# Kernel tuning notes

Hardware: AMD Instinct MI355X
Metric: run time of the kernel (lower is better)

The kernel has to match this reference:

```python
import jax, jax.numpy as jnp
import numpy as np

DIM = 128
WIN = (2, 7, 7)
HEADS = 4
N = WIN[0] * WIN[1] * WIN[2]  # 98
B_ = 2048
NW = 256  # num windows per sample; B_ // NW = batch = 8


def _relative_position_index(win):
    t = np.arange(win[0]); h = np.arange(win[1]); w = np.arange(win[2])
    coords = np.stack(np.meshgrid(t, h, w, indexing='ij'))  # (3, T, H, W)
    cf = coords.reshape(3, -1)  # (3, N)
    rel = cf[:, :, None] - cf[:, None, :]  # (3, N, N)
    rel = rel.transpose(1, 2, 0).copy()
    rel[:, :, 0] += win[0] - 1
    rel[:, :, 1] += win[1] - 1
    rel[:, :, 2] += win[2] - 1
    rel[:, :, 0] *= (2 * win[1] - 1) * (2 * win[2] - 1)
    rel[:, :, 1] *= 2 * win[2] - 1
    return rel.sum(-1).astype(np.int32)  # (N, N)


def setup_inputs() -> dict:
    key = jax.random.key(0)
    ks = jax.random.split(key, 8)
    table_len = (2 * WIN[0] - 1) * (2 * WIN[1] - 1) * (2 * WIN[2] - 1)  # 507
    x = jax.random.normal(ks[0], (B_, N, DIM), dtype=jnp.float32)
    # 0 / -inf style additive mask (use -1e4 as finite -inf)
    u = jax.random.uniform(ks[1], (NW, N, N))
    mask = jnp.where(u < 0.9, 0.0, -1e4).astype(jnp.float32)
    qkv_w = jax.random.normal(ks[2], (3 * DIM, DIM), dtype=jnp.float32) * (DIM ** -0.5)
    qkv_b = jax.random.normal(ks[3], (3 * DIM,), dtype=jnp.float32) * 0.02
    proj_w = jax.random.normal(ks[4], (DIM, DIM), dtype=jnp.float32) * (DIM ** -0.5)
    proj_b = jax.random.normal(ks[5], (DIM,), dtype=jnp.float32) * 0.02
    bias_table = jax.random.normal(ks[6], (table_len, HEADS), dtype=jnp.float32) * 0.02
    rel_index = jnp.asarray(_relative_position_index(WIN))
    return {"x": x, "mask": mask, "qkv_w": qkv_w, "qkv_b": qkv_b,
            "proj_w": proj_w, "proj_b": proj_b, "bias_table": bias_table,
            "rel_index": rel_index}


def reference(x, mask, qkv_w, qkv_b, proj_w, proj_b, bias_table, rel_index):
    Bq, n, c = x.shape
    hd = c // HEADS
    scale = hd ** -0.5
    qkv = x @ qkv_w.T + qkv_b  # (B_, N, 3C)
    qkv = qkv.reshape(Bq, n, 3, HEADS, hd).transpose(2, 0, 3, 1, 4)  # (3, B_, H, N, hd)
    q, k, v = qkv[0] * scale, qkv[1], qkv[2]
    attn = jnp.einsum('bhnd,bhmd->bhnm', q, k)  # (B_, H, N, N)
    bias = bias_table[rel_index.reshape(-1)].reshape(n, n, HEADS)
    attn = attn + bias.transpose(2, 0, 1)[None]  # add (1, H, N, N)
    nW = mask.shape[0]
    attn = attn.reshape(Bq // nW, nW, HEADS, n, n) + mask[None, :, None]
    attn = jax.nn.softmax(attn.reshape(Bq, HEADS, n, n), axis=-1)
    out = jnp.einsum('bhnm,bhmd->bhnd', attn, v)  # (B_, H, N, hd)
    out = out.transpose(0, 2, 1, 3).reshape(Bq, n, c)
    return out @ proj_w.T + proj_b
```

## Files before the change

kernel.cpp:

```cpp
#include <hip/hip_runtime.h>
#include <hip/hip_bf16.h>


#define NTOK 98
#define NN (NTOK * NTOK)
#define SCALE 0.17677669529663687f

typedef short bf16x8 __attribute__((ext_vector_type(8)));
typedef float f32x4 __attribute__((ext_vector_type(4)));
#define MFMA(a, b, c) __builtin_amdgcn_mfma_f32_16x16x32_bf16(a, b, c, 0, 0, 0)

static __device__ __forceinline__ unsigned short f2bf(float f) {
  union { float f; unsigned int i; } x; x.f = f;
  unsigned int u = x.i;
  unsigned int rnd = ((u >> 16) & 1u) + 0x7fffu;
  return (unsigned short)((u + rnd) >> 16);
}
static __device__ __forceinline__ float bf2f(short s) {
  union { unsigned int i; float f; } x;
  x.i = ((unsigned int)(unsigned short)s) << 16;
  return x.f;
}

__global__ void k0_w(const float* __restrict__ qkv_w, const float* __restrict__ proj_w,
                     unsigned short* __restrict__ wqb, unsigned short* __restrict__ wpb) {
  int idx = blockIdx.x * 256 + threadIdx.x;
  if (idx < 49152) wqb[idx] = f2bf(qkv_w[idx]);
  else wpb[idx - 49152] = f2bf(proj_w[idx - 49152]);
}

__global__ void k0b_bm(const float* __restrict__ table, const int* __restrict__ rel,
                       const float* __restrict__ mask, unsigned short* __restrict__ bm) {
  const int wmodh = blockIdx.x, mt = blockIdx.y;
  const int wmod = wmodh >> 2, h = wmodh & 3;
  const int t = threadIdx.x;
  const int lane = t >> 2, reg = t & 3;
  const int quad = lane >> 4, L15 = lane & 15;
  const int row = mt * 16 + quad * 4 + reg;
  bf16x8 v8;
#pragma unroll
  for (int nt = 0; nt < 8; ++nt) {
    float v = -1.0e30f;
    int col = nt * 16 + L15;
    if (nt < 7 && row < NTOK && col < NTOK) {
      int nm = row * NTOK + col;
      v = table[rel[nm] * 4 + h] + mask[(size_t)wmod * NN + nm];
    }
    v8[nt] = (short)f2bf(v);
  }
  *(bf16x8*)&bm[(((size_t)wmodh * 7 + mt) << 11) + (lane << 5) + (reg << 3)] = v8;
}

__global__ __launch_bounds__(256) void k1_qkv(const float* __restrict__ x,
                                              const unsigned short* __restrict__ wqb,
                                              const float* __restrict__ qkv_b,
                                              unsigned short* __restrict__ q,
                                              unsigned short* __restrict__ k,
                                              unsigned short* __restrict__ v) {
  __shared__ unsigned short xt[64 * 136];
  __shared__ unsigned short wt[128 * 136];
  const int t = threadIdx.x;
  const int r0 = blockIdx.x * 64;
  const int wv = t >> 6, lane = t & 63, L15 = lane & 15, quad = lane >> 4;

#pragma unroll
  for (int i = 0; i < 8; ++i) {
    int idx = t + (i << 8);
    int row = idx >> 5, c4 = idx & 31;
    float4 xv = *(const float4*)&x[(size_t)(r0 + row) * 128 + c4 * 4];
    ushort4 pk; pk.x = f2bf(xv.x); pk.y = f2bf(xv.y); pk.z = f2bf(xv.z); pk.w = f2bf(xv.w);
    *(ushort4*)&xt[row * 136 + c4 * 4] = pk;
  }

  bf16x8 af[4];
  bool afLoaded = false;

  for (int g = 0; g < 3; ++g) {
    if (g) __syncthreads();
#pragma unroll
    for (int i = 0; i < 8; ++i) {
      int idx = t + (i << 8);
      int c = idx >> 4, kq = idx & 15;
      *(uint4*)&wt[c * 136 + kq * 8] = ((const uint4*)wqb)[g * 2048 + idx];
    }
    __syncthreads();
    if (!afLoaded) {
      afLoaded = true;
#pragma unroll
      for (int kt = 0; kt < 4; ++kt)
        af[kt] = *(const bf16x8*)&xt[(wv * 16 + L15) * 136 + kt * 32 + quad * 8];
    }

    f32x4 acc[8];
#pragma unroll
    for (int nt = 0; nt < 8; ++nt) {
      f32x4 a = {0.f, 0.f, 0.f, 0.f};
#pragma unroll
      for (int kt = 0; kt < 4; ++kt) {
        bf16x8 bf_ = *(const bf16x8*)&wt[(nt * 16 + L15) * 136 + kt * 32 + quad * 8];
        a = MFMA(af[kt], bf_, a);
      }
      acc[nt] = a;
    }

    unsigned short* dst = (g == 0) ? q : ((g == 1) ? k : v);
    const float sc = (g == 0) ? SCALE : 1.0f;
    float bias[8];
#pragma unroll
    for (int nt = 0; nt < 8; ++nt) bias[nt] = qkv_b[g * 128 + nt * 16 + L15];
#pragma unroll
    for (int reg = 0; reg < 4; ++reg) {
      int R = r0 + wv * 16 + quad * 4 + reg;
      int b = R / NTOK, n = R - b * NTOK;
      size_t base0 = ((size_t)b * 4 * NTOK + n) * 32;
#pragma unroll
      for (int nt = 0; nt < 8; ++nt) {
        int h = nt >> 1, dd = ((nt & 1) << 4) + L15;
        float val = (acc[nt][reg] + bias[nt]) * sc;
        dst[base0 + (size_t)h * (NTOK * 32) + dd] = f2bf(val);
      }
    }
  }
}

__global__ __launch_bounds__(256) void k2_attn(const unsigned short* __restrict__ qg,
                                               const unsigned short* __restrict__ kg,
                                               const unsigned short* __restrict__ vg,
                                               const unsigned short* __restrict__ bm,
                                               unsigned short* __restrict__ og) {
  __shared__ unsigned short sK[112 * 40];
  __shared__ unsigned short sVt[32 * 136];
  __shared__ unsigned short sP[4 * 16 * 136];
  const int t = threadIdx.x;
  const int bh = blockIdx.x, bw = bh >> 2, h = bh & 3;
  const int wmodh = ((bw & 255) << 2) + h;
  const size_t base = (size_t)bh * (NTOK * 32);
  const int wv = t >> 6, lane = t & 63, L15 = lane & 15, quad = lane >> 4;
  unsigned short* myP = sP + wv * (16 * 136);

  for (int i = t; i < 2240; i += 256) ((unsigned int*)sK)[i] = 0;
  for (int j = lane; j < 128; j += 64) {
    int r = j >> 3, cp = j & 7;
    *(unsigned int*)&myP[r * 136 + 112 + cp * 2] = 0;
  }
  __syncthreads();
  for (int i = t; i < 392; i += 256) {
    int row = i >> 2, kq = i & 3;
    *(uint4*)&sK[row * 40 + kq * 8] = ((const uint4*)kg)[(size_t)bh * 392 + i];
  }
  for (int i = t; i < 3136; i += 256) {
    int n = i >> 5, d = i & 31;
    sVt[d * 136 + n] = vg[base + i];
  }
  __syncthreads();

  auto strip = [&](int mt) {
    const unsigned short* bmp = bm + (((size_t)wmodh * 7 + mt) << 11) + (lane << 5);
    bf16x8 bmv[4];
#pragma unroll
    for (int reg = 0; reg < 4; ++reg) bmv[reg] = *(const bf16x8*)&bmp[reg << 3];
    bf16x8 aq = *(const bf16x8*)&qg[base + (size_t)(mt * 16 + L15) * 32 + quad * 8];
    f32x4 s[7];
#pragma unroll
    for (int nt = 0; nt < 7; ++nt) {
      bf16x8 bk = *(const bf16x8*)&sK[(nt * 16 + L15) * 40 + quad * 8];
      f32x4 z = {0.f, 0.f, 0.f, 0.f};
      s[nt] = MFMA(aq, bk, z);
    }
#pragma unroll
    for (int reg = 0; reg < 4; ++reg) {
      float mx = -3.0e38f;
#pragma unroll
      for (int nt = 0; nt < 7; ++nt) {
        float val = s[nt][reg] + bf2f(bmv[reg][nt]);
        s[nt][reg] = val;
        mx = fmaxf(mx, val);
      }
#pragma unroll
      for (int d = 1; d < 16; d <<= 1) mx = fmaxf(mx, __shfl_xor(mx, d, 64));
      float sum = 0.f;
#pragma unroll
      for (int nt = 0; nt < 7; ++nt) {
        float e = __expf(s[nt][reg] - mx);
        s[nt][reg] = e; sum += e;
      }
#pragma unroll
      for (int d = 1; d < 16; d <<= 1) sum += __shfl_xor(sum, d, 64);
      float rs = 1.0f / sum;
#pragma unroll
      for (int nt = 0; nt < 7; ++nt)
        myP[(quad * 4 + reg) * 136 + nt * 16 + L15] = f2bf(s[nt][reg] * rs);
    }
    f32x4 o0 = {0.f, 0.f, 0.f, 0.f}, o1 = {0.f, 0.f, 0.f, 0.f};
#pragma unroll
    for (int kt = 0; kt < 4; ++kt) {
      bf16x8 ap  = *(const bf16x8*)&myP[L15 * 136 + kt * 32 + quad * 8];
      bf16x8 bv0 = *(const bf16x8*)&sVt[L15 * 136 + kt * 32 + quad * 8];
      bf16x8 bv1 = *(const bf16x8*)&sVt[(16 + L15) * 136 + kt * 32 + quad * 8];
      o0 = MFMA(ap, bv0, o0);
      o1 = MFMA(ap, bv1, o1);
    }
#pragma unroll
    for (int reg = 0; reg < 4; ++reg) {
      int n = mt * 16 + quad * 4 + reg;
      if (n < NTOK) {
        size_t ob = ((size_t)bw * NTOK + n) * 128 + h * 32;
        og[ob + L15]      = f2bf(o0[reg]);
        og[ob + 16 + L15] = f2bf(o1[reg]);
      }
    }
  };
  strip(wv * 2);
  if (wv < 3) strip(wv * 2 + 1);
}

__global__ __launch_bounds__(256) void k3_proj(const unsigned short* __restrict__ og,
                                               const unsigned short* __restrict__ wpb,
                                               const float* __restrict__ pb,
                                               float* __restrict__ out) {
  __shared__ unsigned short ot[64 * 136];
  __shared__ unsigned short wt[128 * 136];
  const int t = threadIdx.x;
  const int r0 = blockIdx.x * 64;
  const int wv = t >> 6, lane = t & 63, L15 = lane & 15, quad = lane >> 4;

#pragma unroll
  for (int i = 0; i < 4; ++i) {
    int idx = t + (i << 8);
    int row = idx >> 4, kq = idx & 15;
    *(uint4*)&ot[row * 136 + kq * 8] = ((const uint4*)og)[(size_t)(r0 + row) * 16 + kq];
  }
#pragma unroll
  for (int i = 0; i < 8; ++i) {
    int idx = t + (i << 8);
    int c = idx >> 4, kq = idx & 15;
    *(uint4*)&wt[c * 136 + kq * 8] = ((const uint4*)wpb)[idx];
  }
  __syncthreads();

  bf16x8 af[4];
#pragma unroll
  for (int kt = 0; kt < 4; ++kt)
    af[kt] = *(const bf16x8*)&ot[(wv * 16 + L15) * 136 + kt * 32 + quad * 8];

  f32x4 acc[8];
#pragma unroll
  for (int nt = 0; nt < 8; ++nt) {
    f32x4 a = {0.f, 0.f, 0.f, 0.f};
#pragma unroll
    for (int kt = 0; kt < 4; ++kt) {
      bf16x8 bf_ = *(const bf16x8*)&wt[(nt * 16 + L15) * 136 + kt * 32 + quad * 8];
      a = MFMA(af[kt], bf_, a);
    }
    acc[nt] = a;
  }

  float bias[8];
#pragma unroll
  for (int nt = 0; nt < 8; ++nt) bias[nt] = pb[nt * 16 + L15];
#pragma unroll
  for (int reg = 0; reg < 4; ++reg) {
    size_t R = (size_t)(r0 + wv * 16 + quad * 4 + reg);
#pragma unroll
    for (int nt = 0; nt < 8; ++nt)
      out[R * 128 + nt * 16 + L15] = acc[nt][reg] + bias[nt];
  }
}

extern "C" void kernel_launch(void* const* d_in, const int* in_sizes, int n_in,
                              void* d_out, int out_size, void* d_ws, size_t ws_size,
                              hipStream_t stream) {
  (void)in_sizes; (void)n_in; (void)out_size; (void)ws_size;
  const float* x      = (const float*)d_in[0];
  const float* mask   = (const float*)d_in[1];
  const float* qkv_w  = (const float*)d_in[2];
  const float* qkv_b  = (const float*)d_in[3];
  const float* proj_w = (const float*)d_in[4];
  const float* proj_b = (const float*)d_in[5];
  const float* table  = (const float*)d_in[6];
  const int*   rel    = (const int*)d_in[7];
  float* out = (float*)d_out;

  const size_t QS = (size_t)2048 * 4 * NTOK * 32;
  unsigned short* q   = (unsigned short*)d_ws;
  unsigned short* k   = q + QS;
  unsigned short* v   = k + QS;
  unsigned short* o   = v + QS;
  unsigned short* wqb = o + QS;
  unsigned short* wpb = wqb + 49152;
  unsigned short* bm  = (unsigned short*)d_out;

  k0_w<<<256, 256, 0, stream>>>(qkv_w, proj_w, wqb, wpb);
  k0b_bm<<<dim3(1024, 7), 256, 0, stream>>>(table, rel, mask, bm);
  k1_qkv<<<200704 / 64, 256, 0, stream>>>(x, wqb, qkv_b, q, k, v);
  k2_attn<<<2048 * 4, 256, 0, stream>>>(q, k, v, bm, o);
  k3_proj<<<200704 / 64, 256, 0, stream>>>(o, wpb, proj_b, out);
}
```

Measured before the change: 382.8 us.

## Fold bias into MFMA accumulator, use exp2 softmax without max, defer normalization

```diff
diff --git a/kernel.cpp b/kernel.cpp
--- a/kernel.cpp
+++ b/kernel.cpp
@@ -5,6 +5,7 @@
 #define NTOK 98
 #define NN (NTOK * NTOK)
 #define SCALE 0.17677669529663687f
+#define LOG2E 1.4426950408889634f
 
 typedef short bf16x8 __attribute__((ext_vector_type(8)));
 typedef float f32x4 __attribute__((ext_vector_type(4)));
@@ -16,10 +17,11 @@
   unsigned int rnd = ((u >> 16) & 1u) + 0x7fffu;
   return (unsigned short)((u + rnd) >> 16);
 }
-static __device__ __forceinline__ float bf2f(short s) {
-  union { unsigned int i; float f; } x;
-  x.i = ((unsigned int)(unsigned short)s) << 16;
-  return x.f;
+
+static __device__ __forceinline__ unsigned int cvt_pk_bf16(float lo, float hi) {
+  unsigned int pk;
+  asm("v_cvt_pk_bf16_f32 %0, %1, %2" : "=v"(pk) : "v"(lo), "v"(hi));
+  return pk;
 }
 
 __global__ void k0_w(const float* __restrict__ qkv_w, const float* __restrict__ proj_w,
@@ -30,25 +32,22 @@
 }
 
 __global__ void k0b_bm(const float* __restrict__ table, const int* __restrict__ rel,
-                       const float* __restrict__ mask, unsigned short* __restrict__ bm) {
+                       const float* __restrict__ mask, float* __restrict__ bm) {
   const int wmodh = blockIdx.x, mt = blockIdx.y;
   const int wmod = wmodh >> 2, h = wmodh & 3;
-  const int t = threadIdx.x;
-  const int lane = t >> 2, reg = t & 3;
-  const int quad = lane >> 4, L15 = lane & 15;
-  const int row = mt * 16 + quad * 4 + reg;
-  bf16x8 v8;
-#pragma unroll
-  for (int nt = 0; nt < 8; ++nt) {
+  float* dst = bm + (size_t)(wmodh * 7 + mt) * 1792;
+  for (int i = threadIdx.x; i < 1792; i += 256) {
+    int reg = i & 3, lane = (i >> 2) & 63, nt = i >> 8;
+    int quad = lane >> 4, L15 = lane & 15;
+    int row = mt * 16 + quad * 4 + reg;
+    int col = nt * 16 + L15;
     float v = -1.0e30f;
-    int col = nt * 16 + L15;
-    if (nt < 7 && row < NTOK && col < NTOK) {
+    if (row < NTOK && col < NTOK) {
       int nm = row * NTOK + col;
-      v = table[rel[nm] * 4 + h] + mask[(size_t)wmod * NN + nm];
-    }
-    v8[nt] = (short)f2bf(v);
-  }
-  *(bf16x8*)&bm[(((size_t)wmodh * 7 + mt) << 11) + (lane << 5) + (reg << 3)] = v8;
+      v = (table[rel[nm] * 4 + h] + mask[(size_t)wmod * NN + nm]) * LOG2E;
+    }
+    dst[i] = v;
+  }
 }
 
 __global__ __launch_bounds__(256) void k1_qkv(const float* __restrict__ x,
@@ -104,20 +103,23 @@
     }
 
     unsigned short* dst = (g == 0) ? q : ((g == 1) ? k : v);
-    const float sc = (g == 0) ? SCALE : 1.0f;
-    float bias[8];
-#pragma unroll
-    for (int nt = 0; nt < 8; ++nt) bias[nt] = qkv_b[g * 128 + nt * 16 + L15];
+    const float sc = (g == 0) ? (SCALE * LOG2E) : 1.0f;
+    float bsc[8];
+#pragma unroll
+    for (int nt = 0; nt < 8; ++nt) bsc[nt] = qkv_b[g * 128 + nt * 16 + L15] * sc;
 #pragma unroll
     for (int reg = 0; reg < 4; ++reg) {
       int R = r0 + wv * 16 + quad * 4 + reg;
       int b = R / NTOK, n = R - b * NTOK;
       size_t base0 = ((size_t)b * 4 * NTOK + n) * 32;
 #pragma unroll
-      for (int nt = 0; nt < 8; ++nt) {
-        int h = nt >> 1, dd = ((nt & 1) << 4) + L15;
-        float val = (acc[nt][reg] + bias[nt]) * sc;
-        dst[base0 + (size_t)h * (NTOK * 32) + dd] = f2bf(val);
+      for (int h2 = 0; h2 < 4; ++h2) {
+        float v0 = acc[2 * h2][reg] * sc + bsc[2 * h2];
+        float v1 = acc[2 * h2 + 1][reg] * sc + bsc[2 * h2 + 1];
+        unsigned int pk = cvt_pk_bf16(v0, v1);
+        unsigned short* dp = dst + base0 + (size_t)h2 * (NTOK * 32) + L15;
+        dp[0]  = (unsigned short)pk;
+        dp[16] = (unsigned short)(pk >> 16);
       }
     }
   }
@@ -126,7 +128,7 @@
 __global__ __launch_bounds__(256) void k2_attn(const unsigned short* __restrict__ qg,
                                                const unsigned short* __restrict__ kg,
                                                const unsigned short* __restrict__ vg,
-                                               const unsigned short* __restrict__ bm,
+                                               const float* __restrict__ bm,
                                                unsigned short* __restrict__ og) {
   __shared__ unsigned short sK[112 * 40];
   __shared__ unsigned short sVt[32 * 136];
@@ -148,48 +150,45 @@
     int row = i >> 2, kq = i & 3;
     *(uint4*)&sK[row * 40 + kq * 8] = ((const uint4*)kg)[(size_t)bh * 392 + i];
   }
-  for (int i = t; i < 3136; i += 256) {
-    int n = i >> 5, d = i & 31;
-    sVt[d * 136 + n] = vg[base + i];
+  for (int i = t; i < 392; i += 256) {
+    uint4 w = ((const uint4*)vg)[(size_t)bh * 392 + i];
+    int n = i >> 2, d0 = (i & 3) << 3;
+    const unsigned short* pw = (const unsigned short*)&w;
+#pragma unroll
+    for (int j = 0; j < 8; ++j) sVt[(d0 + j) * 136 + n] = pw[j];
   }
   __syncthreads();
 
   auto strip = [&](int mt) {
-    const unsigned short* bmp = bm + (((size_t)wmodh * 7 + mt) << 11) + (lane << 5);
-    bf16x8 bmv[4];
-#pragma unroll
-    for (int reg = 0; reg < 4; ++reg) bmv[reg] = *(const bf16x8*)&bmp[reg << 3];
+    const float* bmp = bm + (size_t)(wmodh * 7 + mt) * 1792 + (lane << 2);
     bf16x8 aq = *(const bf16x8*)&qg[base + (size_t)(mt * 16 + L15) * 32 + quad * 8];
     f32x4 s[7];
 #pragma unroll
     for (int nt = 0; nt < 7; ++nt) {
+      f32x4 c = *(const f32x4*)&bmp[nt << 8];
       bf16x8 bk = *(const bf16x8*)&sK[(nt * 16 + L15) * 40 + quad * 8];
-      f32x4 z = {0.f, 0.f, 0.f, 0.f};
-      s[nt] = MFMA(aq, bk, z);
-    }
+      s[nt] = MFMA(aq, bk, c);
+    }
+    float rsv[4];
 #pragma unroll
     for (int reg = 0; reg < 4; ++reg) {
-      float mx = -3.0e38f;
+      float sum = 0.f;
 #pragma unroll
       for (int nt = 0; nt < 7; ++nt) {
-        float val = s[nt][reg] + bf2f(bmv[reg][nt]);
-        s[nt][reg] = val;
-        mx = fmaxf(mx, val);
-      }
-#pragma unroll
-      for (int d = 1; d < 16; d <<= 1) mx = fmaxf(mx, __shfl_xor(mx, d, 64));
-      float sum = 0.f;
-#pragma unroll
-      for (int nt = 0; nt < 7; ++nt) {
-        float e = __expf(s[nt][reg] - mx);
+        float e = __builtin_amdgcn_exp2f(s[nt][reg]);
         s[nt][reg] = e; sum += e;
       }
 #pragma unroll
       for (int d = 1; d < 16; d <<= 1) sum += __shfl_xor(sum, d, 64);
-      float rs = 1.0f / sum;
-#pragma unroll
-      for (int nt = 0; nt < 7; ++nt)
-        myP[(quad * 4 + reg) * 136 + nt * 16 + L15] = f2bf(s[nt][reg] * rs);
+      rsv[reg] = __builtin_amdgcn_rcpf(sum);
+      unsigned short* pr = myP + (quad * 4 + reg) * 136 + L15;
+#pragma unroll
+      for (int p = 0; p < 4; ++p) {
+        int n1 = (p < 3) ? 2 * p + 1 : 2 * p;
+        unsigned int pk = cvt_pk_bf16(s[2 * p][reg], s[n1][reg]);
+        pr[2 * p * 16] = (unsigned short)pk;
+        if (p < 3) pr[n1 * 16] = (unsigned short)(pk >> 16);
+      }
     }
     f32x4 o0 = {0.f, 0.f, 0.f, 0.f}, o1 = {0.f, 0.f, 0.f, 0.f};
 #pragma unroll
@@ -205,8 +204,10 @@
       int n = mt * 16 + quad * 4 + reg;
       if (n < NTOK) {
         size_t ob = ((size_t)bw * NTOK + n) * 128 + h * 32;
-        og[ob + L15]      = f2bf(o0[reg]);
-        og[ob + 16 + L15] = f2bf(o1[reg]);
+        float a0 = o0[reg] * rsv[reg], a1 = o1[reg] * rsv[reg];
+        unsigned int pk = cvt_pk_bf16(a0, a1);
+        og[ob + L15]      = (unsigned short)pk;
+        og[ob + 16 + L15] = (unsigned short)(pk >> 16);
       }
     }
   };
@@ -288,7 +289,7 @@
   unsigned short* o   = v + QS;
   unsigned short* wqb = o + QS;
   unsigned short* wpb = wqb + 49152;
-  unsigned short* bm  = (unsigned short*)d_out;
+  float* bm = (float*)d_out;
 
   k0_w<<<256, 256, 0, stream>>>(qkv_w, proj_w, wqb, wpb);
   k0b_bm<<<dim3(1024, 7), 256, 0, stream>>>(table, rel, mask, bm);
```

New measurement: 374.2 us. 2.3% less time.
